# Kernel tuning notes

Measured on AMD Instinct MI355X. Metric: run time of the kernel, lower is better.

Reference implementation:

```python
import jax, jax.numpy as jnp
import numpy as np

N_NODES = 4
EPS = 1e-12


def gcn_conv(x, edge_index, W, b):
    B, N, _ = x.shape
    loop = jnp.arange(N)
    src = jnp.concatenate([edge_index[0], loop])
    dst = jnp.concatenate([edge_index[1], loop])
    deg = jnp.zeros((N,), x.dtype).at[dst].add(1.0)  # in-degree incl. self loops (>=1)
    dinv = jax.lax.rsqrt(deg)
    norm = dinv[src] * dinv[dst]                      # [E+N]
    h = jnp.einsum('bnf,fo->bno', x, W)               # transform first (out < ... ok)
    msgs = h[:, src, :] * norm[None, :, None]         # gather + edge weight
    out = jnp.zeros((B, N, W.shape[1]), x.dtype).at[:, dst, :].add(msgs)  # scatter-add
    return out + b


def sage_conv(x, edge_index, Wl, bl, Wr):
    # PyG SAGEConv(aggr='mean', normalize=True): out = lin_l(mean_j x_j) + lin_r(x_i), l2-normalized
    B, N, F = x.shape
    src, dst = edge_index[0], edge_index[1]
    cnt = jnp.zeros((N,), x.dtype).at[dst].add(1.0)
    cnt = jnp.maximum(cnt, 1.0)
    agg = jnp.zeros((B, N, F), x.dtype).at[:, dst, :].add(x[:, src, :])
    agg = agg / cnt[None, :, None]                    # mean neighbor aggregation
    out = jnp.einsum('bnf,fo->bno', agg, Wl) + bl + jnp.einsum('bnf,fo->bno', x, Wr)
    nrm = jnp.sqrt(jnp.sum(out * out, axis=-1, keepdims=True))
    return out / jnp.maximum(nrm, EPS)


def setup_inputs() -> dict:
    key = jax.random.key(0)
    ks = jax.random.split(key, 16)
    B, N, Cin, Cout = 32768, N_NODES, 64, 10
    E = 12

    def glorot(k, fi, fo):
        s = (6.0 / (fi + fo)) ** 0.5
        return jax.random.uniform(k, (fi, fo), jnp.float32, -s, s)

    x = jax.random.normal(ks[0], (B, N, Cin), jnp.float32)
    edge_index = jax.random.randint(ks[1], (2, E), 0, N, jnp.int64)
    inp = {
        'x': x, 'edge_index': edge_index,
        'W1': glorot(ks[2], Cin, 1024), 'b1': jnp.zeros((1024,), jnp.float32),
        'Wl2': glorot(ks[3], 1024, 512), 'bl2': jnp.zeros((512,), jnp.float32), 'Wr2': glorot(ks[4], 1024, 512),
        'Wl3': glorot(ks[5], 512, 256), 'bl3': jnp.zeros((256,), jnp.float32), 'Wr3': glorot(ks[6], 512, 256),
        'Wl4': glorot(ks[7], 256, 256), 'bl4': jnp.zeros((256,), jnp.float32), 'Wr4': glorot(ks[8], 256, 256),
        'Wfc': glorot(ks[9], N * 256, Cout), 'bfc': jnp.zeros((Cout,), jnp.float32),
    }
    return inp


def reference(x, edge_index, W1, b1, Wl2, bl2, Wr2, Wl3, bl3, Wr3, Wl4, bl4, Wr4, Wfc, bfc):
    h = jax.nn.relu(gcn_conv(x, edge_index, W1, b1))
    h = jax.nn.relu(sage_conv(h, edge_index, Wl2, bl2, Wr2))
    h = jax.nn.relu(sage_conv(h, edge_index, Wl3, bl3, Wr3))
    h = jax.nn.relu(sage_conv(h, edge_index, Wl4, bl4, Wr4))
    h = h.reshape(h.shape[0], -1)                     # [B, 4*256]
    logits = h @ Wfc + bfc
    return jax.nn.softmax(logits, axis=-1)
```

## Files before the change

### kernel.cpp

```cpp
#include <hip/hip_runtime.h>
#include <stdint.h>
#include <math.h>

typedef __bf16 bf16;
typedef __attribute__((ext_vector_type(8))) __bf16 bf16x8;
typedef __attribute__((ext_vector_type(16))) float f32x16;

#define AS1 __attribute__((address_space(1)))
#define AS3 __attribute__((address_space(3)))

__device__ __forceinline__ void glds16(const void* g, void* l) {
    __builtin_amdgcn_global_load_lds((const AS1 uint32_t*)g, (AS3 uint32_t*)l, 16, 0, 0);
}


__global__ void k_setup(const int* __restrict__ ei, float* __restrict__ gmat) {
    if (threadIdx.x != 0 || blockIdx.x != 0) return;
    bool is64 = true;
    for (int i = 0; i < 12; i++) if (ei[2 * i + 1] != 0) { is64 = false; break; }
    int src[12], dst[12];
    for (int e = 0; e < 12; e++) {
        if (is64) { src[e] = ei[2 * e]; dst[e] = ei[24 + 2 * e]; }
        else      { src[e] = ei[e];     dst[e] = ei[12 + e]; }
    }
    float deg[4] = {1.f, 1.f, 1.f, 1.f};
    for (int e = 0; e < 12; e++) deg[dst[e]] += 1.f;
    float dinv[4];
    for (int n = 0; n < 4; n++) dinv[n] = 1.f / sqrtf(deg[n]);
    float A[16];
    for (int i = 0; i < 16; i++) A[i] = 0.f;
    for (int e = 0; e < 12; e++) A[dst[e] * 4 + src[e]] += dinv[src[e]] * dinv[dst[e]];
    for (int n = 0; n < 4; n++) A[n * 4 + n] += dinv[n] * dinv[n];
    float cnt[4] = {0.f, 0.f, 0.f, 0.f};
    for (int e = 0; e < 12; e++) cnt[dst[e]] += 1.f;
    for (int n = 0; n < 4; n++) cnt[n] = fmaxf(cnt[n], 1.f);
    float Mm[16];
    for (int i = 0; i < 16; i++) Mm[i] = 0.f;
    for (int e = 0; e < 12; e++) Mm[dst[e] * 4 + src[e]] += 1.f;
    for (int n = 0; n < 4; n++)
        for (int m = 0; m < 4; m++) Mm[n * 4 + m] /= cnt[n];
    for (int i = 0; i < 16; i++) { gmat[i] = A[i]; gmat[16 + i] = Mm[i]; }
}

__global__ __launch_bounds__(256) void wtransF(const float* __restrict__ W, int K,
                                               int N, bf16* __restrict__ Wt) {
    int a = blockIdx.x * 256 + threadIdx.x;
    if (a >= N * K) return;
    int j = a & 7, c64 = (a >> 3) & 63, tile = a >> 9;
    int m32 = c64 & 31, kh = c64 >> 5;
    int TK = K >> 4;
    int rblk = tile / TK, ks = tile - rblk * TK;
    int n = rblk * 32 + m32, k = ks * 16 + kh * 8 + j;
    Wt[a] = (bf16)W[(size_t)k * N + n];
}

__global__ __launch_bounds__(256) void wtransI(const float* __restrict__ Wl,
                                               const float* __restrict__ Wr,
                                               int K, int F, bf16* __restrict__ Bt) {
    int a = blockIdx.x * 256 + threadIdx.x;
    if (a >= 2 * F * K) return;
    int j = a & 7, c64 = (a >> 3) & 63, tile = a >> 9;
    int m32 = c64 & 31, kh = c64 >> 5;
    int TK = K >> 4;
    int rblk = tile / TK, ks = tile - rblk * TK;
    int n = rblk * 32 + m32, k = ks * 16 + kh * 8 + j;
    int f = n >> 1;
    float v = (n & 1) ? Wr[(size_t)k * F + f] : Wl[(size_t)k * F + f];
    Bt[a] = (bf16)v;
}

__global__ __launch_bounds__(256) void cast_x(const float4* __restrict__ x,
                                              bf16x8* __restrict__ out) {
    int i = blockIdx.x * 256 + threadIdx.x;
    int c64 = i & 63, m32 = c64 & 31, kh = c64 >> 5;
    int tile = i >> 6, RB = tile >> 2, ks = tile & 3;
    int row = RB * 32 + m32;
    int fb4 = ks * 4 + kh * 2;
    float4 a = x[(size_t)row * 16 + fb4], b = x[(size_t)row * 16 + fb4 + 1];
    bf16x8 o;
    o[0] = (bf16)a.x; o[1] = (bf16)a.y; o[2] = (bf16)a.z; o[3] = (bf16)a.w;
    o[4] = (bf16)b.x; o[5] = (bf16)b.y; o[6] = (bf16)b.z; o[7] = (bf16)b.w;
    out[i] = o;
}

__global__ __launch_bounds__(256) void k_zero(float4* __restrict__ p, int n4) {
    int i = blockIdx.x * 256 + threadIdx.x;
    if (i < n4) p[i] = make_float4(0.f, 0.f, 0.f, 0.f);
}

__global__ __launch_bounds__(256, 2) void gemm_mfma(
    const bf16* __restrict__ A, int K,
    const bf16* __restrict__ Bt,
    const float* __restrict__ bias,
    bf16* __restrict__ out, int N, int mode,
    const float* __restrict__ gm, float* __restrict__ ssq,
    const float* __restrict__ insq) {
    __shared__ bf16 sA[8192];
    __shared__ bf16 sB[16384];
    const int t = threadIdx.x;
    const int lane = t & 63;
    const int w = t >> 6;
    const int wr = w >> 1, wc = w & 1;
    const int lin = blockIdx.x + gridDim.x * blockIdx.y;
    const int C = gridDim.x;
    const int cls = lin & 7;
    const int s0 = lin >> 3;
    const int rpc = gridDim.y >> 3;
    const int sy = s0 / C;
    const int row0 = (cls * rpc + sy) * 128;
    const int col0 = (s0 - sy * C) * 256;
    const int m32 = lane & 31;
    const int kh = lane >> 5;

    f32x16 acc[2][4] = {};

    const int TK = K >> 4;
    const size_t tA  = ((size_t)(row0 >> 5) + w) * TK;
    const size_t tB0 = ((size_t)(col0 >> 5) + w) * TK;
    const size_t tB1 = ((size_t)(col0 >> 5) + w + 4) * TK;
    const int le = lane * 8;

    for (int kb = 0; kb < K; kb += 64) {
        int kt = kb >> 4;
#pragma unroll
        for (int s = 0; s < 4; s++) {
            glds16(A  + (tA  + kt + s) * 512 + le, &sA[(s * 4 + w) * 512]);
            glds16(Bt + (tB0 + kt + s) * 512 + le, &sB[(s * 8 + w) * 512]);
            glds16(Bt + (tB1 + kt + s) * 512 + le, &sB[(s * 8 + w + 4) * 512]);
        }
        __syncthreads();
#pragma unroll
        for (int s = 0; s < 4; s++) {
            bf16x8 af[2], bfr[4];
#pragma unroll
            for (int i = 0; i < 2; i++)
                af[i] = *(const bf16x8*)&sA[(s * 4 + 2 * wr + i) * 512 + le];
#pragma unroll
            for (int j = 0; j < 4; j++)
                bfr[j] = *(const bf16x8*)&sB[(s * 8 + 4 * wc + j) * 512 + le];
#pragma unroll
            for (int i = 0; i < 2; i++)
#pragma unroll
                for (int j = 0; j < 4; j++)
                    acc[i][j] = __builtin_amdgcn_mfma_f32_32x32x16_bf16(af[i], bfr[j], acc[i][j], 0, 0, 0);
        }
        __syncthreads();
    }

    float g[16];
#pragma unroll
    for (int q = 0; q < 16; q++) g[q] = gm[q];

    if (mode == 1) {
        const int Tn = N >> 4;
#pragma unroll
        for (int i = 0; i < 2; i++) {
            size_t RBo = (size_t)(row0 >> 5) + 2 * wr + i;
#pragma unroll
            for (int j = 0; j < 4; j++) {
                int c = col0 + (4 * wc + j) * 32 + m32;
                size_t tbase = (RBo * Tn + (c >> 4)) * 512;
                int coff = ((c >> 3) & 1) * 32;
                int cj = c & 7;
                float bsv = bias[c];
#pragma unroll
                for (int q = 0; q < 4; q++) {
#pragma unroll
                    for (int n = 0; n < 4; n++) {
                        float v = g[n * 4 + 0] * acc[i][j][q * 4 + 0] +
                                  g[n * 4 + 1] * acc[i][j][q * 4 + 1] +
                                  g[n * 4 + 2] * acc[i][j][q * 4 + 2] +
                                  g[n * 4 + 3] * acc[i][j][q * 4 + 3] + bsv;
                        out[tbase + (size_t)(coff + 4 * kh + 8 * q + n) * 8 + cj] =
                            (bf16)fmaxf(v, 0.f);
                    }
                }
            }
        }
    } else {
        const int F = N >> 1;
        const int Tf = F >> 4;
        const bool ev = ((m32 & 1) == 0);
        const bool hasin = (insq != nullptr);
#pragma unroll
        for (int i = 0; i < 2; i++) {
            size_t RBo = (size_t)(row0 >> 5) + 2 * wr + i;
            int rbAbs = row0 + (2 * wr + i) * 32 + 4 * kh;
#pragma unroll
            for (int q = 0; q < 4; q++) {
                float invq[4] = {1.f, 1.f, 1.f, 1.f};
                if (hasin) {
#pragma unroll
                    for (int n = 0; n < 4; n++)
                        invq[n] = 1.f / fmaxf(sqrtf(insq[rbAbs + 8 * q + n]), 1e-12f);
                }
                float ssql[4] = {0.f, 0.f, 0.f, 0.f};
#pragma unroll
                for (int j = 0; j < 4; j++) {
                    int c = col0 + (4 * wc + j) * 32 + m32;
                    int f = c >> 1;
                    size_t tbase = (RBo * Tf + (f >> 4)) * 512;
                    int foff = ((f >> 3) & 1) * 32;
                    int fj = f & 7;
                    float bsv = bias[f];
                    float a_s[4];
#pragma unroll
                    for (int k2 = 0; k2 < 4; k2++)
                        a_s[k2] = acc[i][j][q * 4 + k2] * invq[k2];
                    float mine[4];
                    if (ev) {
#pragma unroll
                        for (int n = 0; n < 4; n++)
                            mine[n] = g[n * 4 + 0] * a_s[0] +
                                      g[n * 4 + 1] * a_s[1] +
                                      g[n * 4 + 2] * a_s[2] +
                                      g[n * 4 + 3] * a_s[3];
                    } else {
#pragma unroll
                        for (int n = 0; n < 4; n++) mine[n] = a_s[n];
                    }
#pragma unroll
                    for (int n = 0; n < 4; n++) {
                        float oth = __shfl_xor(mine[n], 1);
                        float tot = mine[n] + oth + bsv;
                        ssql[n] += tot * tot;
                        if (ev)
                            out[tbase + (size_t)(foff + 4 * kh + 8 * q + n) * 8 + fj] =
                                (bf16)fmaxf(tot, 0.f);
                    }
                }
#pragma unroll
                for (int n = 0; n < 4; n++) {
                    float v = ssql[n];
                    v += __shfl_xor(v, 1); v += __shfl_xor(v, 2);
                    v += __shfl_xor(v, 4); v += __shfl_xor(v, 8);
                    v += __shfl_xor(v, 16);
                    ssql[n] = v;
                }
                if (m32 == 0) {
#pragma unroll
                    for (int n = 0; n < 4; n++)
                        atomicAdd(&ssq[rbAbs + 8 * q + n], ssql[n] * 0.5f);
                }
            }
        }
    }
}

__global__ __launch_bounds__(256) void fc_softmax(const bf16x8* __restrict__ h,
                                                  const float* __restrict__ ssq4,
                                                  const float* __restrict__ Wfc,
                                                  const float* __restrict__ bfc,
                                                  float* __restrict__ outp) {
    __shared__ float WT[10][1024];
    int t = threadIdx.x;
    for (int i = t; i < 10240; i += 256) { int o = i % 10, k = i / 10; WT[o][k] = Wfc[i]; }
    __syncthreads();
    int wid = t >> 6, lane = t & 63;
    size_t e = (size_t)blockIdx.x * 4 + wid;
    size_t eb8 = e >> 3;
    int eo = (int)(e & 7);
    int ks = lane & 15, node = lane >> 4;
    float inv = 1.f / fmaxf(sqrtf(ssq4[e * 4 + node]), 1e-12f);
    float acc[10];
#pragma unroll
    for (int o = 0; o < 10; o++) acc[o] = 0.f;
#pragma unroll
    for (int jj = 0; jj < 2; jj++) {
        size_t ch = (eb8 * 16 + ks) * 64 + jj * 32 + eo * 4 + node;
        bf16x8 v = h[ch];
        float f[8];
#pragma unroll
        for (int c = 0; c < 8; c++) f[c] = fmaxf((float)v[c] * inv, 0.f);
        int k0 = node * 256 + ks * 16 + jj * 8;
#pragma unroll
        for (int o = 0; o < 10; o++) {
            const float* wr = &WT[o][k0];
            float s = 0.f;
#pragma unroll
            for (int c = 0; c < 8; c++) s += f[c] * wr[c];
            acc[o] += s;
        }
    }
#pragma unroll
    for (int o = 0; o < 10; o++) {
        float v = acc[o];
        v += __shfl_xor(v, 32); v += __shfl_xor(v, 16); v += __shfl_xor(v, 8);
        v += __shfl_xor(v, 4);  v += __shfl_xor(v, 2);  v += __shfl_xor(v, 1);
        acc[o] = v + bfc[o];
    }
    float mx = acc[0];
#pragma unroll
    for (int o = 1; o < 10; o++) mx = fmaxf(mx, acc[o]);
    float sum = 0.f, p[10];
#pragma unroll
    for (int o = 0; o < 10; o++) { p[o] = expf(acc[o] - mx); sum += p[o]; }
    float inv2 = 1.f / sum;
    if (lane < 10) outp[e * 10 + lane] = p[lane] * inv2;
}

extern "C" void kernel_launch(void* const* d_in, const int* in_sizes, int n_in,
                              void* d_out, int out_size, void* d_ws, size_t ws_size,
                              hipStream_t stream) {
    const float* x   = (const float*)d_in[0];
    const int*   ei  = (const int*)d_in[1];
    const float* W1  = (const float*)d_in[2];
    const float* b1  = (const float*)d_in[3];
    const float* Wl2 = (const float*)d_in[4];
    const float* bl2 = (const float*)d_in[5];
    const float* Wr2 = (const float*)d_in[6];
    const float* Wl3 = (const float*)d_in[7];
    const float* bl3 = (const float*)d_in[8];
    const float* Wr3 = (const float*)d_in[9];
    const float* Wl4 = (const float*)d_in[10];
    const float* bl4 = (const float*)d_in[11];
    const float* Wr4 = (const float*)d_in[12];
    const float* Wfc = (const float*)d_in[13];
    const float* bfc = (const float*)d_in[14];
    float* out = (float*)d_out;

    const int B = 32768;
    char* base = (char*)d_ws;
    float* gmat = (float*)base;
    bf16* Wt1 = (bf16*)(base + 4096);
    bf16* Wt2 = Wt1 + 1024 * 64;
    bf16* Wt3 = Wt2 + 1024 * 1024;
    bf16* Wt4 = Wt3 + 512 * 512;
    float* ssqb = (float*)(Wt4 + 512 * 256);
    char* sl  = (char*)(ssqb + 12 * B);
    size_t fixed = (size_t)(sl - base);

    int Bs = B;
    while (Bs > 512 && fixed + (size_t)Bs * 12800 > ws_size) Bs >>= 1;
    int nslice = B / Bs;
    int M = Bs * 4;

    bf16* R0 = (bf16*)sl;
    bf16* R1 = R0 + (size_t)Bs * 256;
    bf16* R2 = R1 + (size_t)Bs * 4096;

    hipLaunchKernelGGL(k_setup, dim3(1), dim3(64), 0, stream, ei, gmat);
    hipLaunchKernelGGL(wtransF, dim3((1024 * 64 + 255) / 256), dim3(256), 0, stream,
                       W1, 64, 1024, Wt1);
    hipLaunchKernelGGL(wtransI, dim3((1024 * 1024 + 255) / 256), dim3(256), 0, stream,
                       Wl2, Wr2, 1024, 512, Wt2);
    hipLaunchKernelGGL(wtransI, dim3((512 * 512 + 255) / 256), dim3(256), 0, stream,
                       Wl3, Wr3, 512, 256, Wt3);
    hipLaunchKernelGGL(wtransI, dim3((512 * 256 + 255) / 256), dim3(256), 0, stream,
                       Wl4, Wr4, 256, 256, Wt4);
    hipLaunchKernelGGL(k_zero, dim3((3 * B + 255) / 256), dim3(256), 0, stream,
                       (float4*)ssqb, 3 * B);

    for (int s = 0; s < nslice; s++) {
        const float* xs = x + (size_t)s * Bs * 256;
        float* ssqs = ssqb + (size_t)s * 3 * M;
        hipLaunchKernelGGL(cast_x, dim3(Bs / 8), dim3(256), 0, stream,
                           (const float4*)xs, (bf16x8*)R0);
        hipLaunchKernelGGL(gemm_mfma, dim3(4, M / 128), dim3(256), 0, stream,
                           R0, 64, Wt1, b1, R1, 1024, 1, gmat, (float*)nullptr,
                           (const float*)nullptr);
        hipLaunchKernelGGL(gemm_mfma, dim3(4, M / 128), dim3(256), 0, stream,
                           R1, 1024, Wt2, bl2, R2, 1024, 2, gmat + 16, ssqs,
                           (const float*)nullptr);
        hipLaunchKernelGGL(gemm_mfma, dim3(2, M / 128), dim3(256), 0, stream,
                           R2, 512, Wt3, bl3, R1, 512, 2, gmat + 16, ssqs + M,
                           (const float*)ssqs);
        hipLaunchKernelGGL(gemm_mfma, dim3(2, M / 128), dim3(256), 0, stream,
                           R1, 256, Wt4, bl4, R2, 512, 2, gmat + 16, ssqs + 2 * M,
                           (const float*)(ssqs + M));
        hipLaunchKernelGGL(fc_softmax, dim3(Bs / 4), dim3(256), 0, stream,
                           (const bf16x8*)R2, ssqs + 2 * M, Wfc, bfc,
                           out + (size_t)s * Bs * 10);
    }
}
```

Measured before the change: 913.2 us.

## Fuse input cast into first GEMM and merge setup kernels into one launch

The first GEMM (mode 1) now reads fp32 x directly, converts it to bf16 in registers and writes it into shared memory, which removes the separate cast_x kernel and its intermediate buffer. The setup, weight-transpose and zeroing kernels are merged into a single block-partitioned k_prep launch to cut launch overhead. The fused A load uses ordinary global loads plus an LDS store instead of the asynchronous global-to-LDS path, which could expose load latency in the first GEMM. It also shrinks the workspace needed per slice.

Result: no change. 927.6 us (+1.6%).

```diff
diff --git a/kernel.cpp b/kernel.cpp
--- a/kernel.cpp
+++ b/kernel.cpp
@@ -14,8 +14,53 @@
 }
 
 
-__global__ void k_setup(const int* __restrict__ ei, float* __restrict__ gmat) {
-    if (threadIdx.x != 0 || blockIdx.x != 0) return;
+__device__ __forceinline__ void wtransF_body(int a, const float* __restrict__ W,
+                                             int K, int N, bf16* __restrict__ Wt) {
+    int j = a & 7, c64 = (a >> 3) & 63, tile = a >> 9;
+    int m32 = c64 & 31, kh = c64 >> 5;
+    int TK = K >> 4;
+    int rblk = tile / TK, ks = tile - rblk * TK;
+    int n = rblk * 32 + m32, k = ks * 16 + kh * 8 + j;
+    Wt[a] = (bf16)W[(size_t)k * N + n];
+}
+
+__device__ __forceinline__ void wtransI_body(int a, const float* __restrict__ Wl,
+                                             const float* __restrict__ Wr,
+                                             int K, int F, bf16* __restrict__ Bt) {
+    int j = a & 7, c64 = (a >> 3) & 63, tile = a >> 9;
+    int m32 = c64 & 31, kh = c64 >> 5;
+    int TK = K >> 4;
+    int rblk = tile / TK, ks = tile - rblk * TK;
+    int n = rblk * 32 + m32, k = ks * 16 + kh * 8 + j;
+    int f = n >> 1;
+    float v = (n & 1) ? Wr[(size_t)k * F + f] : Wl[(size_t)k * F + f];
+    Bt[a] = (bf16)v;
+}
+
+__global__ __launch_bounds__(256) void k_prep(
+    const int* __restrict__ ei, float* __restrict__ gmat,
+    const float* __restrict__ W1,
+    const float* __restrict__ Wl2, const float* __restrict__ Wr2,
+    const float* __restrict__ Wl3, const float* __restrict__ Wr3,
+    const float* __restrict__ Wl4, const float* __restrict__ Wr4,
+    bf16* __restrict__ Wt1, bf16* __restrict__ Wt2,
+    bf16* __restrict__ Wt3, bf16* __restrict__ Wt4,
+    float4* __restrict__ ssqz) {
+    int b = blockIdx.x, t = threadIdx.x;
+    if (b < 384) {
+        int i = b * 256 + t;
+        if (i < 3 * 32768) ssqz[i] = make_float4(0.f, 0.f, 0.f, 0.f);
+        return;
+    }
+    b -= 384;
+    if (b < 256) { wtransF_body(b * 256 + t, W1, 64, 1024, Wt1); return; }
+    b -= 256;
+    if (b < 4096) { wtransI_body(b * 256 + t, Wl2, Wr2, 1024, 512, Wt2); return; }
+    b -= 4096;
+    if (b < 1024) { wtransI_body(b * 256 + t, Wl3, Wr3, 512, 256, Wt3); return; }
+    b -= 1024;
+    if (b < 512) { wtransI_body(b * 256 + t, Wl4, Wr4, 256, 256, Wt4); return; }
+    if (t != 0) return;
     bool is64 = true;
     for (int i = 0; i < 12; i++) if (ei[2 * i + 1] != 0) { is64 = false; break; }
     int src[12], dst[12];
@@ -40,52 +85,6 @@
     for (int n = 0; n < 4; n++)
         for (int m = 0; m < 4; m++) Mm[n * 4 + m] /= cnt[n];
     for (int i = 0; i < 16; i++) { gmat[i] = A[i]; gmat[16 + i] = Mm[i]; }
-}
-
-__global__ __launch_bounds__(256) void wtransF(const float* __restrict__ W, int K,
-                                               int N, bf16* __restrict__ Wt) {
-    int a = blockIdx.x * 256 + threadIdx.x;
-    if (a >= N * K) return;
-    int j = a & 7, c64 = (a >> 3) & 63, tile = a >> 9;
-    int m32 = c64 & 31, kh = c64 >> 5;
-    int TK = K >> 4;
-    int rblk = tile / TK, ks = tile - rblk * TK;
-    int n = rblk * 32 + m32, k = ks * 16 + kh * 8 + j;
-    Wt[a] = (bf16)W[(size_t)k * N + n];
-}
-
-__global__ __launch_bounds__(256) void wtransI(const float* __restrict__ Wl,
-                                               const float* __restrict__ Wr,
-                                               int K, int F, bf16* __restrict__ Bt) {
-    int a = blockIdx.x * 256 + threadIdx.x;
-    if (a >= 2 * F * K) return;
-    int j = a & 7, c64 = (a >> 3) & 63, tile = a >> 9;
-    int m32 = c64 & 31, kh = c64 >> 5;
-    int TK = K >> 4;
-    int rblk = tile / TK, ks = tile - rblk * TK;
-    int n = rblk * 32 + m32, k = ks * 16 + kh * 8 + j;
-    int f = n >> 1;
-    float v = (n & 1) ? Wr[(size_t)k * F + f] : Wl[(size_t)k * F + f];
-    Bt[a] = (bf16)v;
-}
-
-__global__ __launch_bounds__(256) void cast_x(const float4* __restrict__ x,
-                                              bf16x8* __restrict__ out) {
-    int i = blockIdx.x * 256 + threadIdx.x;
-    int c64 = i & 63, m32 = c64 & 31, kh = c64 >> 5;
-    int tile = i >> 6, RB = tile >> 2, ks = tile & 3;
-    int row = RB * 32 + m32;
-    int fb4 = ks * 4 + kh * 2;
-    float4 a = x[(size_t)row * 16 + fb4], b = x[(size_t)row * 16 + fb4 + 1];
-    bf16x8 o;
-    o[0] = (bf16)a.x; o[1] = (bf16)a.y; o[2] = (bf16)a.z; o[3] = (bf16)a.w;
-    o[4] = (bf16)b.x; o[5] = (bf16)b.y; o[6] = (bf16)b.z; o[7] = (bf16)b.w;
-    out[i] = o;
-}
-
-__global__ __launch_bounds__(256) void k_zero(float4* __restrict__ p, int n4) {
-    int i = blockIdx.x * 256 + threadIdx.x;
-    if (i < n4) p[i] = make_float4(0.f, 0.f, 0.f, 0.f);
 }
 
 __global__ __launch_bounds__(256, 2) void gemm_mfma(
@@ -122,11 +121,32 @@
 
     for (int kb = 0; kb < K; kb += 64) {
         int kt = kb >> 4;
-#pragma unroll
-        for (int s = 0; s < 4; s++) {
-            glds16(A  + (tA  + kt + s) * 512 + le, &sA[(s * 4 + w) * 512]);
-            glds16(Bt + (tB0 + kt + s) * 512 + le, &sB[(s * 8 + w) * 512]);
-            glds16(Bt + (tB1 + kt + s) * 512 + le, &sB[(s * 8 + w + 4) * 512]);
+        if (mode == 1) {
+            const float4* xf = (const float4*)A;
+            int r = row0 + w * 32 + m32;
+#pragma unroll
+            for (int s = 0; s < 4; s++) {
+                float4 av = xf[(size_t)r * 16 + s * 4 + kh * 2];
+                float4 bv = xf[(size_t)r * 16 + s * 4 + kh * 2 + 1];
+                bf16x8 o;
+                o[0] = (bf16)av.x; o[1] = (bf16)av.y;
+                o[2] = (bf16)av.z; o[3] = (bf16)av.w;
+                o[4] = (bf16)bv.x; o[5] = (bf16)bv.y;
+                o[6] = (bf16)bv.z; o[7] = (bf16)bv.w;
+                *(bf16x8*)&sA[(s * 4 + w) * 512 + le] = o;
+            }
+#pragma unroll
+            for (int s = 0; s < 4; s++) {
+                glds16(Bt + (tB0 + kt + s) * 512 + le, &sB[(s * 8 + w) * 512]);
+                glds16(Bt + (tB1 + kt + s) * 512 + le, &sB[(s * 8 + w + 4) * 512]);
+            }
+        } else {
+#pragma unroll
+            for (int s = 0; s < 4; s++) {
+                glds16(A  + (tA  + kt + s) * 512 + le, &sA[(s * 4 + w) * 512]);
+                glds16(Bt + (tB0 + kt + s) * 512 + le, &sB[(s * 8 + w) * 512]);
+                glds16(Bt + (tB1 + kt + s) * 512 + le, &sB[(s * 8 + w + 4) * 512]);
+            }
         }
         __syncthreads();
 #pragma unroll
@@ -331,34 +351,23 @@
     size_t fixed = (size_t)(sl - base);
 
     int Bs = B;
-    while (Bs > 512 && fixed + (size_t)Bs * 12800 > ws_size) Bs >>= 1;
+    while (Bs > 512 && fixed + (size_t)Bs * 12288 > ws_size) Bs >>= 1;
     int nslice = B / Bs;
     int M = Bs * 4;
 
-    bf16* R0 = (bf16*)sl;
-    bf16* R1 = R0 + (size_t)Bs * 256;
+    bf16* R1 = (bf16*)sl;
     bf16* R2 = R1 + (size_t)Bs * 4096;
 
-    hipLaunchKernelGGL(k_setup, dim3(1), dim3(64), 0, stream, ei, gmat);
-    hipLaunchKernelGGL(wtransF, dim3((1024 * 64 + 255) / 256), dim3(256), 0, stream,
-                       W1, 64, 1024, Wt1);
-    hipLaunchKernelGGL(wtransI, dim3((1024 * 1024 + 255) / 256), dim3(256), 0, stream,
-                       Wl2, Wr2, 1024, 512, Wt2);
-    hipLaunchKernelGGL(wtransI, dim3((512 * 512 + 255) / 256), dim3(256), 0, stream,
-                       Wl3, Wr3, 512, 256, Wt3);
-    hipLaunchKernelGGL(wtransI, dim3((512 * 256 + 255) / 256), dim3(256), 0, stream,
-                       Wl4, Wr4, 256, 256, Wt4);
-    hipLaunchKernelGGL(k_zero, dim3((3 * B + 255) / 256), dim3(256), 0, stream,
-                       (float4*)ssqb, 3 * B);
+    hipLaunchKernelGGL(k_prep, dim3(6273), dim3(256), 0, stream,
+                       ei, gmat, W1, Wl2, Wr2, Wl3, Wr3, Wl4, Wr4,
+                       Wt1, Wt2, Wt3, Wt4, (float4*)ssqb);
 
     for (int s = 0; s < nslice; s++) {
         const float* xs = x + (size_t)s * Bs * 256;
         float* ssqs = ssqb + (size_t)s * 3 * M;
-        hipLaunchKernelGGL(cast_x, dim3(Bs / 8), dim3(256), 0, stream,
-                           (const float4*)xs, (bf16x8*)R0);
         hipLaunchKernelGGL(gemm_mfma, dim3(4, M / 128), dim3(256), 0, stream,
-                           R0, 64, Wt1, b1, R1, 1024, 1, gmat, (float*)nullptr,
-                           (const float*)nullptr);
+                           (const bf16*)xs, 64, Wt1, b1, R1, 1024, 1, gmat,
+                           (float*)nullptr, (const float*)nullptr);
         hipLaunchKernelGGL(gemm_mfma, dim3(4, M / 128), dim3(256), 0, stream,
                            R1, 1024, Wt2, bl2, R2, 1024, 2, gmat + 16, ssqs,
                            (const float*)nullptr);
```
